# Optimization experiments

Hardware: AMD Instinct MI355X
Metric: run time of the kernel (lower is better)

Reference implementation:

```python
import jax, jax.numpy as jnp
import numpy as np

NH, HS, K = 32, 2048, 16
HD = HS // NH
B, L = 4, 2048
EPS = 1e-6

def _ln(x, gamma, beta):
    mu = x.mean(-1, keepdims=True)
    var = x.var(-1, keepdims=True)  # ddof=0 == torch unbiased=False
    return gamma * ((x - mu) / jnp.sqrt(var + EPS)) + beta

def _ln_fused_l2_bwd(x, target, gamma, beta):
    D = x.shape[-1]
    mu = x.mean(-1, keepdims=True)
    std = jnp.sqrt(x.var(-1, keepdims=True) + EPS)
    xh = (x - mu) / std
    gxh = (gamma * xh + beta - target) * gamma
    return (D * gxh - gxh.sum(-1, keepdims=True) - xh * (gxh * xh).sum(-1, keepdims=True)) / (D * std)

def setup_inputs() -> dict:
    key = jax.random.key(0)
    ks = jax.random.split(key, 8)
    s = 0.02
    return {
        'hidden_states': jax.random.normal(ks[0], (B, L, HS), jnp.float32),
        'position_ids': jnp.tile(jnp.arange(L, dtype=jnp.int32)[None], (B, 1)),
        'q_w': jax.random.normal(ks[1], (HS, HS), jnp.float32) * s,
        'k_w': jax.random.normal(ks[2], (HS, HS), jnp.float32) * s,
        'v_w': jax.random.normal(ks[3], (HS, HS), jnp.float32) * s,
        'o_w': jax.random.normal(ks[4], (HS, HS), jnp.float32) * s,
        'W1': jax.random.normal(ks[5], (NH, HD, HD), jnp.float32) * s,
        'b1': jnp.zeros((NH, 1, HD), jnp.float32),
        'ttt_norm_weight': jnp.ones((NH, HD), jnp.float32),
        'ttt_norm_bias': jnp.zeros((NH, HD), jnp.float32),
        'ttt_lr_weight': jax.random.normal(ks[6], (NH, 1, HS), jnp.float32) * s,
        'ttt_lr_bias': jnp.zeros((NH, 1), jnp.float32),
        'learnable_token_idx': jnp.zeros((K,), jnp.float32),
        'post_norm_weight': jnp.ones((HS,), jnp.float32),
        'post_norm_bias': jnp.zeros((HS,), jnp.float32),
    }

def _forward(hidden_states, q_w, k_w, v_w, o_w, W1, b1, ttt_norm_weight,
             ttt_norm_bias, ttt_lr_weight, ttt_lr_bias, learnable_token_idx,
             post_norm_weight, post_norm_bias):
    Bb, Ll, _ = hidden_states.shape
    NM = Ll // K

    def proj_heads(w):
        return (hidden_states @ w.T).reshape(Bb, Ll, NH, HD).transpose(0, 2, 1, 3)

    XQ = proj_heads(q_w).reshape(Bb, NH, NM, K, HD)
    XK = proj_heads(k_w).reshape(Bb, NH, NM, K, HD)
    XV = proj_heads(v_w).reshape(Bb, NH, NM, K, HD)
    X = hidden_states.reshape(Bb, NM, K, HS)

    # eta: learned per-token lr gate, [B,nh,NM,K,K]
    ttt_lr = jnp.einsum('bnkc,hdc->bhnkd', X, ttt_lr_weight) + ttt_lr_bias.reshape(1, NH, 1, 1, 1)
    ttt_lr_eta = jax.nn.sigmoid(ttt_lr).transpose(0, 1, 2, 4, 3) / HD  # ttt_base_lr = 1.0
    token_idx = jnp.clip(1.0 / jnp.arange(1, K + 1, dtype=jnp.float32) + learnable_token_idx, 0.0, None)
    eta = token_idx.reshape(1, 1, 1, K, 1) * ttt_lr_eta

    ln_w = ttt_norm_weight.reshape(NH, 1, HD)
    ln_b = ttt_norm_bias.reshape(NH, 1, HD)

    def step(carry, x):
        W1_s, b1_s = carry                 # [B,nh,hd,hd], [B,nh,1,hd]
        xq, xk, xv, eta_mb = x             # [B,nh,K,hd], eta_mb [B,nh,K,K]
        Z1 = xk @ W1_s + b1_s
        grad = _ln_fused_l2_bwd(Z1, xv - xk, ln_w, ln_b)
        Attn1 = jnp.tril(xq @ xk.swapaxes(-1, -2))
        b1_bar = b1_s - jnp.tril(eta_mb) @ grad
        Z1_bar = xq @ W1_s - (eta_mb * Attn1) @ grad + b1_bar
        last_eta = eta_mb[:, :, -1, :, None]  # [B,nh,K,1]
        W1_new = W1_s - (last_eta * xk).swapaxes(-1, -2) @ grad
        b1_new = b1_s - jnp.sum(last_eta * grad, axis=-2, keepdims=True)
        out = xq + _ln(Z1_bar, ln_w, ln_b)
        return (W1_new, b1_new), out

    init = (jnp.tile(W1[None], (Bb, 1, 1, 1)), jnp.tile(b1[None], (Bb, 1, 1, 1)))
    xs = (XQ.transpose(2, 0, 1, 3, 4), XK.transpose(2, 0, 1, 3, 4),
          XV.transpose(2, 0, 1, 3, 4), eta.transpose(2, 0, 1, 3, 4))
    _, ys = jax.lax.scan(step, init, xs)          # [NM,B,nh,K,hd]
    out = ys.transpose(1, 0, 3, 2, 4).reshape(Bb, Ll, HS)
    out = _ln(out, post_norm_weight, post_norm_bias)  # post_norm (eps 1e-6)
    return out @ o_w.T

def reference(hidden_states, position_ids, q_w, k_w, v_w, o_w, W1, b1,
              ttt_norm_weight, ttt_norm_bias, ttt_lr_weight, ttt_lr_bias,
              learnable_token_idx, post_norm_weight, post_norm_bias):
    del position_ids  # unused in the shown forward (rope never applied)
    return _forward(hidden_states, q_w, k_w, v_w, o_w, W1, b1, ttt_norm_weight,
                    ttt_norm_bias, ttt_lr_weight, ttt_lr_bias, learnable_token_idx,
                    post_norm_weight, post_norm_bias)
```

## Files before the change

kernel.cpp:

```cpp
#include <hip/hip_runtime.h>

typedef unsigned short u16;
typedef unsigned int u32;
typedef __bf16 bf16_t;
typedef bf16_t bf16x8 __attribute__((ext_vector_type(8)));
typedef float f32x4 __attribute__((ext_vector_type(4)));
typedef u16 u16x8 __attribute__((ext_vector_type(8)));

#define B_   4
#define L_   2048
#define HS_  2048
#define NH_  32
#define HD_  64
#define KK_  16
#define NM_  128
#define M_   (B_*L_)

__device__ __forceinline__ u16 f2bf(float f) {
  unsigned u = __float_as_uint(f);
  u += 0x7FFFu + ((u >> 16) & 1u);
  return (u16)(u >> 16);
}
__device__ __forceinline__ float bf2f(u16 u) {
  return __uint_as_float(((unsigned)u) << 16);
}
__device__ __forceinline__ f32x4 vshfl_xor(f32x4 v, int m) {
  f32x4 r;
  r[0] = __shfl_xor(v[0], m, 64); r[1] = __shfl_xor(v[1], m, 64);
  r[2] = __shfl_xor(v[2], m, 64); r[3] = __shfl_xor(v[3], m, 64);
  return r;
}

__global__ __launch_bounds__(256) void cast_f32_bf16(const float* __restrict__ in,
                                                     u16* __restrict__ out, int n) {
  int i = (blockIdx.x * 256 + threadIdx.x) * 8;
  if (i >= n) return;
  float4 a = *(const float4*)(in + i);
  float4 b = *(const float4*)(in + i + 4);
  u16x8 o;
  o[0]=f2bf(a.x); o[1]=f2bf(a.y); o[2]=f2bf(a.z); o[3]=f2bf(a.w);
  o[4]=f2bf(b.x); o[5]=f2bf(b.y); o[6]=f2bf(b.z); o[7]=f2bf(b.w);
  *(u16x8*)(out + i) = o;
}

#define BM 128
#define BN 128
#define BK 32
#define LDT 40

template <bool BF16OUT>
__global__ __launch_bounds__(256) void gemm_nt(const u16* __restrict__ A,
                                               const u16* __restrict__ Bt,
                                               void* __restrict__ Cv,
                                               int M, int N, int K) {
  __shared__ u16 As[BM * LDT];
  __shared__ u16 Bs[BN * LDT];
  int tid  = threadIdx.x;
  int lane = tid & 63, wave = tid >> 6;
  int quad = lane >> 4, l16 = lane & 15;
  int bM = blockIdx.x * BM, bN = blockIdx.y * BN;
  int wM = (wave >> 1) * 64, wN = (wave & 1) * 64;
  int r0 = tid >> 2, c0 = (tid & 3) * 8;
  const u16* Ap = A + (size_t)bM * K;
  const u16* Bp = Bt + (size_t)bN * K;
  f32x4 acc[4][4] = {};
  u16x8 pa0 = *(const u16x8*)(Ap + (size_t)r0 * K + c0);
  u16x8 pa1 = *(const u16x8*)(Ap + (size_t)(r0 + 64) * K + c0);
  u16x8 pb0 = *(const u16x8*)(Bp + (size_t)r0 * K + c0);
  u16x8 pb1 = *(const u16x8*)(Bp + (size_t)(r0 + 64) * K + c0);
  int nk = K / BK;
  for (int kt = 0; kt < nk; ++kt) {
    *(u16x8*)&As[r0 * LDT + c0]        = pa0;
    *(u16x8*)&As[(r0 + 64) * LDT + c0] = pa1;
    *(u16x8*)&Bs[r0 * LDT + c0]        = pb0;
    *(u16x8*)&Bs[(r0 + 64) * LDT + c0] = pb1;
    __syncthreads();
    if (kt + 1 < nk) {
      int k0 = (kt + 1) * BK + c0;
      pa0 = *(const u16x8*)(Ap + (size_t)r0 * K + k0);
      pa1 = *(const u16x8*)(Ap + (size_t)(r0 + 64) * K + k0);
      pb0 = *(const u16x8*)(Bp + (size_t)r0 * K + k0);
      pb1 = *(const u16x8*)(Bp + (size_t)(r0 + 64) * K + k0);
    }
    bf16x8 af[4], bfr[4];
#pragma unroll
    for (int i = 0; i < 4; ++i) {
      u16x8 t = *(const u16x8*)&As[(wM + i * 16 + l16) * LDT + quad * 8];
      af[i] = __builtin_bit_cast(bf16x8, t);
    }
#pragma unroll
    for (int j = 0; j < 4; ++j) {
      u16x8 t = *(const u16x8*)&Bs[(wN + j * 16 + l16) * LDT + quad * 8];
      bfr[j] = __builtin_bit_cast(bf16x8, t);
    }
#pragma unroll
    for (int i = 0; i < 4; ++i) {
#pragma unroll
      for (int j = 0; j < 4; ++j)
        acc[i][j] = __builtin_amdgcn_mfma_f32_16x16x32_bf16(af[i], bfr[j], acc[i][j], 0, 0, 0);
    }
    __syncthreads();
  }
#pragma unroll
  for (int i = 0; i < 4; ++i) {
#pragma unroll
    for (int j = 0; j < 4; ++j) {
      int row = bM + wM + i * 16 + quad * 4;
      int col = bN + wN + j * 16 + l16;
      if (BF16OUT) {
        u16* cp = (u16*)Cv + (size_t)row * N + col;
#pragma unroll
        for (int r = 0; r < 4; ++r) cp[(size_t)r * N] = f2bf(acc[i][j][r]);
      } else {
        float* cp = (float*)Cv + (size_t)row * N + col;
#pragma unroll
        for (int r = 0; r < 4; ++r) cp[(size_t)r * N] = acc[i][j][r];
      }
    }
  }
}

__global__ __launch_bounds__(256) void sig_kernel(const u16* __restrict__ hsb,
                                                  const u16* __restrict__ lrwb,
                                                  const float* __restrict__ lrb,
                                                  float* __restrict__ Sig) {
  __shared__ u16 Bs[32 * LDT];
  int tid = threadIdx.x;
  int lane = tid & 63, wave = tid >> 6;
  int quad = lane >> 4, l16 = lane & 15;
  int m0 = blockIdx.x * 64 + wave * 16;
  f32x4 acc0 = {}, acc1 = {};
  for (int kt = 0; kt < HS_ / BK; ++kt) {
    int k0 = kt * BK;
    if (tid < 128) {
      int r = tid >> 2, c8 = (tid & 3) * 8;
      *(u16x8*)&Bs[r * LDT + c8] = *(const u16x8*)(lrwb + (size_t)r * HS_ + k0 + c8);
    }
    __syncthreads();
    u16x8 ta = *(const u16x8*)(hsb + (size_t)(m0 + l16) * HS_ + k0 + quad * 8);
    u16x8 t0 = *(const u16x8*)&Bs[l16 * LDT + quad * 8];
    u16x8 t1 = *(const u16x8*)&Bs[(16 + l16) * LDT + quad * 8];
    bf16x8 af  = __builtin_bit_cast(bf16x8, ta);
    bf16x8 bf0 = __builtin_bit_cast(bf16x8, t0);
    bf16x8 bf1 = __builtin_bit_cast(bf16x8, t1);
    acc0 = __builtin_amdgcn_mfma_f32_16x16x32_bf16(af, bf0, acc0, 0, 0, 0);
    acc1 = __builtin_amdgcn_mfma_f32_16x16x32_bf16(af, bf1, acc1, 0, 0, 0);
    __syncthreads();
  }
#pragma unroll
  for (int j = 0; j < 2; ++j) {
    f32x4 a = j ? acc1 : acc0;
    int h = j * 16 + l16;
    float bias = lrb[h];
#pragma unroll
    for (int r = 0; r < 4; ++r) {
      int m = m0 + quad * 4 + r;
      float v = a[r] + bias;
      float s = (1.f / (1.f + expf(-v))) * (1.f / 64.f);
      Sig[(size_t)m * NH_ + h] = s;
    }
  }
}

__global__ __launch_bounds__(64, 1) void ttt_scan_wave(
    const u16* __restrict__ XQ, const u16* __restrict__ XK, const u16* __restrict__ XV,
    const float* __restrict__ Sig, const float* __restrict__ W1_0, const float* __restrict__ b1_0,
    const float* __restrict__ lnw, const float* __restrict__ lnb, const float* __restrict__ lti,
    float* __restrict__ Y) {
  __shared__ u16 W1t[64 * 72];
  __shared__ u16 gradT[64 * 40];
  __shared__ u16 coefA[16 * 40];
  __shared__ u16 xkT[64 * 40];
  __shared__ float diffS[16 * 68];
  __shared__ float xqF[16 * 68];

  int lane = threadIdx.x;
  int quad = lane >> 4, l16 = lane & 15;
  int bh = blockIdx.x, b = bh >> 5, h = bh & 31;

  {
    u32* p = (u32*)gradT; for (int i = lane; i < 1280; i += 64) p[i] = 0;
    u32* q = (u32*)coefA; for (int i = lane; i < 320;  i += 64) q[i] = 0;
    u32* s = (u32*)xkT;   for (int i = lane; i < 1280; i += 64) s[i] = 0;
  }

  f32x4 master[4][4];
  {
    const float* wsrc = W1_0 + (size_t)h * 4096;
#pragma unroll
    for (int c = 0; c < 4; ++c) {
      const float* wc = wsrc + (size_t)(c * 16 + l16) * 64 + quad * 4;
#pragma unroll
      for (int a = 0; a < 4; ++a)
#pragma unroll
        for (int r = 0; r < 4; ++r) master[a][c][r] = wc[a * 16 + r];
    }
  }
#pragma unroll
  for (int a = 0; a < 4; ++a)
#pragma unroll
    for (int c = 0; c < 4; ++c)
#pragma unroll
      for (int r = 0; r < 4; ++r)
        W1t[(a * 16 + quad * 4 + r) * 72 + c * 16 + l16] = f2bf(master[a][c][r]);

  f32x4 b1r, gam, bet;
#pragma unroll
  for (int c = 0; c < 4; ++c) {
    b1r[c] = b1_0[h * 64 + c * 16 + l16];
    gam[c] = lnw[h * 64 + c * 16 + l16];
    bet[c] = lnb[h * 64 + c * 16 + l16];
  }
  f32x4 tok4;
#pragma unroll
  for (int r = 0; r < 4; ++r) {
    int kk = quad * 4 + r;
    tok4[r] = fmaxf(1.0f / (float)(kk + 1) + lti[kk], 0.0f);
  }
  float tok15 = fmaxf(1.0f / 16.0f + lti[15], 0.0f);

  size_t gb  = ((size_t)(b * L_ + l16)) * HS_ + h * HD_ + quad * 8;
  size_t sgb = (size_t)(b * L_ + l16) * NH_ + h;

  u16x8 cxk[2], cxq[2], cxv[2];
  float csig;
#pragma unroll
  for (int kc = 0; kc < 2; ++kc) {
    cxk[kc] = *(const u16x8*)(XK + gb + kc * 32);
    cxq[kc] = *(const u16x8*)(XQ + gb + kc * 32);
    cxv[kc] = *(const u16x8*)(XV + gb + kc * 32);
  }
  csig = Sig[sgb];

  for (int n = 0; n < NM_; ++n) {
    bf16x8 fw[4][2];
#pragma unroll
    for (int cb = 0; cb < 4; ++cb)
#pragma unroll
      for (int kc = 0; kc < 2; ++kc)
        fw[cb][kc] = __builtin_bit_cast(bf16x8,
            *(const u16x8*)&W1t[(cb * 16 + l16) * 72 + kc * 32 + quad * 8]);

#pragma unroll
    for (int kc = 0; kc < 2; ++kc) {
      float dv[8], qv[8];
#pragma unroll
      for (int j = 0; j < 8; ++j) {
        dv[j] = bf2f(cxv[kc][j]) - bf2f(cxk[kc][j]);
        qv[j] = bf2f(cxq[kc][j]);
      }
      float4 d0 = {dv[0], dv[1], dv[2], dv[3]}, d1 = {dv[4], dv[5], dv[6], dv[7]};
      float4 q0 = {qv[0], qv[1], qv[2], qv[3]}, q1 = {qv[4], qv[5], qv[6], qv[7]};
      *(float4*)&diffS[l16 * 68 + kc * 32 + quad * 8]     = d0;
      *(float4*)&diffS[l16 * 68 + kc * 32 + quad * 8 + 4] = d1;
      *(float4*)&xqF[l16 * 68 + kc * 32 + quad * 8]       = q0;
      *(float4*)&xqF[l16 * 68 + kc * 32 + quad * 8 + 4]   = q1;
#pragma unroll
      for (int j = 0; j < 8; ++j)
        xkT[(kc * 32 + quad * 8 + j) * 40 + l16] = f2bf(-tok15 * bf2f(cxk[kc][j]));
    }
    f32x4 ssig;
#pragma unroll
    for (int r = 0; r < 4; ++r) ssig[r] = __shfl(csig, quad * 4 + r, 64);

    bf16x8 fxk[2], fxq[2];
#pragma unroll
    for (int kc = 0; kc < 2; ++kc) {
      fxk[kc] = __builtin_bit_cast(bf16x8, cxk[kc]);
      fxq[kc] = __builtin_bit_cast(bf16x8, cxq[kc]);
    }

    if (n + 1 < NM_) {
      size_t g = gb + (size_t)(n + 1) * KK_ * HS_;
#pragma unroll
      for (int kc = 0; kc < 2; ++kc) {
        cxk[kc] = *(const u16x8*)(XK + g + kc * 32);
        cxq[kc] = *(const u16x8*)(XQ + g + kc * 32);
        cxv[kc] = *(const u16x8*)(XV + g + kc * 32);
      }
      csig = Sig[sgb + (size_t)(n + 1) * KK_ * NH_];
    }

    f32x4 z1[4] = {}, zq[4] = {}, at = {};
#pragma unroll
    for (int kc = 0; kc < 2; ++kc) {
      at = __builtin_amdgcn_mfma_f32_16x16x32_bf16(fxq[kc], fxk[kc], at, 0, 0, 0);
#pragma unroll
      for (int cb = 0; cb < 4; ++cb) {
        z1[cb] = __builtin_amdgcn_mfma_f32_16x16x32_bf16(fxk[kc], fw[cb][kc], z1[cb], 0, 0, 0);
        zq[cb] = __builtin_amdgcn_mfma_f32_16x16x32_bf16(fxq[kc], fw[cb][kc], zq[cb], 0, 0, 0);
      }
    }

#pragma unroll
    for (int r = 0; r < 4; ++r) {
      int kk = quad * 4 + r;
      float cc = (l16 <= kk) ? tok4[r] * (1.0f + at[r]) : 0.0f;
      coefA[kk * 40 + l16] = f2bf(-cc);
    }

    f32x4 dd[4], xqr[4];
#pragma unroll
    for (int cb = 0; cb < 4; ++cb)
#pragma unroll
      for (int r = 0; r < 4; ++r) {
        dd[cb][r]  = diffS[(quad * 4 + r) * 68 + cb * 16 + l16];
        xqr[cb][r] = xqF[(quad * 4 + r) * 68 + cb * 16 + l16];
      }

    f32x4 s1 = {}, s2 = {};
#pragma unroll
    for (int cb = 0; cb < 4; ++cb) {
#pragma unroll
      for (int r = 0; r < 4; ++r) z1[cb][r] += b1r[cb];
      s1 = s1 + z1[cb];
      s2 = s2 + z1[cb] * z1[cb];
    }
#pragma unroll
    for (int m = 1; m <= 8; m <<= 1) { s1 = s1 + vshfl_xor(s1, m); s2 = s2 + vshfl_xor(s2, m); }
    f32x4 mu, rstd;
#pragma unroll
    for (int r = 0; r < 4; ++r) {
      mu[r] = s1[r] * (1.0f / 64.0f);
      float var = s2[r] * (1.0f / 64.0f) - mu[r] * mu[r];
      rstd[r] = 1.0f / sqrtf(var + 1e-6f);
    }

    f32x4 xh[4], gxh[4], t1v = {}, t2v = {};
#pragma unroll
    for (int cb = 0; cb < 4; ++cb) {
#pragma unroll
      for (int r = 0; r < 4; ++r) {
        xh[cb][r]  = (z1[cb][r] - mu[r]) * rstd[r];
        gxh[cb][r] = (gam[cb] * xh[cb][r] + bet[cb] - dd[cb][r]) * gam[cb];
      }
      t1v = t1v + gxh[cb];
      t2v = t2v + gxh[cb] * xh[cb];
    }
#pragma unroll
    for (int m = 1; m <= 8; m <<= 1) { t1v = t1v + vshfl_xor(t1v, m); t2v = t2v + vshfl_xor(t2v, m); }

    f32x4 bsum = {};
#pragma unroll
    for (int cb = 0; cb < 4; ++cb) {
      float sg[4];
#pragma unroll
      for (int r = 0; r < 4; ++r) {
        float g = (64.0f * gxh[cb][r] - t1v[r] - xh[cb][r] * t2v[r]) * (rstd[r] * (1.0f / 64.0f));
        sg[r] = ssig[r] * g;
      }
      u32 p0 = (u32)f2bf(sg[0]) | ((u32)f2bf(sg[1]) << 16);
      u32 p1 = (u32)f2bf(sg[2]) | ((u32)f2bf(sg[3]) << 16);
      *(u32*)&gradT[(cb * 16 + l16) * 40 + quad * 4]     = p0;
      *(u32*)&gradT[(cb * 16 + l16) * 40 + quad * 4 + 2] = p1;
      bsum[cb] = sg[0] + sg[1] + sg[2] + sg[3];
    }
    bsum = bsum + vshfl_xor(bsum, 16);
    bsum = bsum + vshfl_xor(bsum, 32);

    bf16x8 fA = __builtin_bit_cast(bf16x8, *(const u16x8*)&coefA[l16 * 40 + quad * 8]);
    bf16x8 fG[4], fX[4];
#pragma unroll
    for (int cb = 0; cb < 4; ++cb) {
      fG[cb] = __builtin_bit_cast(bf16x8, *(const u16x8*)&gradT[(cb * 16 + l16) * 40 + quad * 8]);
      fX[cb] = __builtin_bit_cast(bf16x8, *(const u16x8*)&xkT[(cb * 16 + l16) * 40 + quad * 8]);
    }

    f32x4 zb[4];
#pragma unroll
    for (int cb = 0; cb < 4; ++cb) {
      zb[cb] = __builtin_amdgcn_mfma_f32_16x16x32_bf16(fA, fG[cb], zq[cb], 0, 0, 0);
#pragma unroll
      for (int r = 0; r < 4; ++r) zb[cb][r] += b1r[cb];
    }

#pragma unroll
    for (int a = 0; a < 4; ++a)
#pragma unroll
      for (int c = 0; c < 4; ++c)
        master[a][c] = __builtin_amdgcn_mfma_f32_16x16x32_bf16(fG[a], fX[c], master[a][c], 0, 0, 0);
#pragma unroll
    for (int c = 0; c < 4; ++c) b1r[c] -= tok15 * bsum[c];

    f32x4 w1s = {}, w2s = {};
#pragma unroll
    for (int cb = 0; cb < 4; ++cb) { w1s = w1s + zb[cb]; w2s = w2s + zb[cb] * zb[cb]; }
#pragma unroll
    for (int m = 1; m <= 8; m <<= 1) { w1s = w1s + vshfl_xor(w1s, m); w2s = w2s + vshfl_xor(w2s, m); }
#pragma unroll
    for (int r = 0; r < 4; ++r) {
      float mu2 = w1s[r] * (1.0f / 64.0f);
      float var2 = w2s[r] * (1.0f / 64.0f) - mu2 * mu2;
      float rstd2 = 1.0f / sqrtf(var2 + 1e-6f);
      float* yp = Y + ((size_t)(b * L_ + n * KK_ + quad * 4 + r)) * HS_ + h * HD_ + l16;
#pragma unroll
      for (int cb = 0; cb < 4; ++cb)
        yp[cb * 16] = xqr[cb][r] + gam[cb] * ((zb[cb][r] - mu2) * rstd2) + bet[cb];
    }

#pragma unroll
    for (int a = 0; a < 4; ++a)
#pragma unroll
      for (int c = 0; c < 4; ++c)
#pragma unroll
        for (int r = 0; r < 4; ++r)
          W1t[(a * 16 + quad * 4 + r) * 72 + c * 16 + l16] = f2bf(master[a][c][r]);
  }
}

__global__ __launch_bounds__(256) void postnorm(const float* __restrict__ Yin,
                                                const float* __restrict__ w,
                                                const float* __restrict__ bb,
                                                u16* __restrict__ Yn) {
  __shared__ float red[8];
  int row = blockIdx.x, tid = threadIdx.x;
  const float* x = Yin + (size_t)row * HS_ + tid * 8;
  float4 v0 = *(const float4*)(x);
  float4 v1 = *(const float4*)(x + 4);
  float s  = v0.x + v0.y + v0.z + v0.w + v1.x + v1.y + v1.z + v1.w;
  float ss = v0.x*v0.x + v0.y*v0.y + v0.z*v0.z + v0.w*v0.w
           + v1.x*v1.x + v1.y*v1.y + v1.z*v1.z + v1.w*v1.w;
#pragma unroll
  for (int m = 32; m > 0; m >>= 1) { s += __shfl_xor(s, m, 64); ss += __shfl_xor(ss, m, 64); }
  int wave = tid >> 6, lane = tid & 63;
  if (lane == 0) { red[wave] = s; red[4 + wave] = ss; }
  __syncthreads();
  float S  = red[0] + red[1] + red[2] + red[3];
  float SS = red[4] + red[5] + red[6] + red[7];
  float mu = S * (1.f / 2048.f);
  float var = SS * (1.f / 2048.f) - mu * mu;
  float rstd = 1.f / sqrtf(var + 1e-6f);
  const float* wp = w + tid * 8;
  const float* bp = bb + tid * 8;
  float vals[8] = {v0.x, v0.y, v0.z, v0.w, v1.x, v1.y, v1.z, v1.w};
  u16x8 o;
#pragma unroll
  for (int t = 0; t < 8; ++t) o[t] = f2bf(wp[t] * ((vals[t] - mu) * rstd) + bp[t]);
  *(u16x8*)(Yn + (size_t)row * HS_ + tid * 8) = o;
}

extern "C" void kernel_launch(void* const* d_in, const int* in_sizes, int n_in,
                              void* d_out, int out_size, void* d_ws, size_t ws_size,
                              hipStream_t stream) {
  (void)in_sizes; (void)n_in; (void)out_size; (void)ws_size;
  const float* hidden = (const float*)d_in[0];
  const float* q_w = (const float*)d_in[2];
  const float* k_w = (const float*)d_in[3];
  const float* v_w = (const float*)d_in[4];
  const float* o_w = (const float*)d_in[5];
  const float* W1  = (const float*)d_in[6];
  const float* b1i = (const float*)d_in[7];
  const float* lnw = (const float*)d_in[8];
  const float* lnb = (const float*)d_in[9];
  const float* lrw = (const float*)d_in[10];
  const float* lrb = (const float*)d_in[11];
  const float* lti = (const float*)d_in[12];
  const float* pnw = (const float*)d_in[13];
  const float* pnb = (const float*)d_in[14];
  float* out = (float*)d_out;

  char* w = (char*)d_ws;
  u16* hsb  = (u16*)w;  w += (size_t)16777216 * 2;
  u16* wb   = (u16*)w;  w += (size_t)4194304 * 2;
  u16* lrwb = (u16*)w;  w += (size_t)65536 * 2;
  u16* XQb  = (u16*)w;  w += (size_t)16777216 * 2;
  u16* XKb  = (u16*)w;  w += (size_t)16777216 * 2;
  u16* XVb  = (u16*)w;  w += (size_t)16777216 * 2;
  float* Sg = (float*)w; w += (size_t)M_ * NH_ * 4;
  u16* Yn = hsb;

  cast_f32_bf16<<<8192, 256, 0, stream>>>(hidden, hsb, 16777216);
  cast_f32_bf16<<<32, 256, 0, stream>>>(lrw, lrwb, 65536);

  sig_kernel<<<128, 256, 0, stream>>>(hsb, lrwb, lrb, Sg);

  dim3 gg(M_ / BM, HS_ / BN);
  cast_f32_bf16<<<2048, 256, 0, stream>>>(q_w, wb, 4194304);
  gemm_nt<true><<<gg, 256, 0, stream>>>(hsb, wb, XQb, M_, HS_, HS_);
  cast_f32_bf16<<<2048, 256, 0, stream>>>(k_w, wb, 4194304);
  gemm_nt<true><<<gg, 256, 0, stream>>>(hsb, wb, XKb, M_, HS_, HS_);
  cast_f32_bf16<<<2048, 256, 0, stream>>>(v_w, wb, 4194304);
  gemm_nt<true><<<gg, 256, 0, stream>>>(hsb, wb, XVb, M_, HS_, HS_);

  ttt_scan_wave<<<128, 64, 0, stream>>>(XQb, XKb, XVb, Sg, W1, b1i, lnw, lnb, lti, out);

  postnorm<<<8192, 256, 0, stream>>>(out, pnw, pnb, Yn);

  cast_f32_bf16<<<2048, 256, 0, stream>>>(o_w, wb, 4194304);
  gemm_nt<false><<<gg, 256, 0, stream>>>(Yn, wb, out, M_, HS_, HS_);
}
```

Baseline: 1.053 ms.

## Keep TTT scan state in registers with 16x16x16 MFMA layout and DPP reductions

Result: faster. 893.0 us (-15.2%).

```diff
diff --git a/kernel.cpp b/kernel.cpp
--- a/kernel.cpp
+++ b/kernel.cpp
@@ -3,9 +3,12 @@
 typedef unsigned short u16;
 typedef unsigned int u32;
 typedef __bf16 bf16_t;
+typedef bf16_t bf16x4 __attribute__((ext_vector_type(4)));
 typedef bf16_t bf16x8 __attribute__((ext_vector_type(8)));
 typedef float f32x4 __attribute__((ext_vector_type(4)));
+typedef u16 u16x4 __attribute__((ext_vector_type(4)));
 typedef u16 u16x8 __attribute__((ext_vector_type(8)));
+typedef short s16x4 __attribute__((ext_vector_type(4)));
 
 #define B_   4
 #define L_   2048
@@ -24,11 +27,38 @@
 __device__ __forceinline__ float bf2f(u16 u) {
   return __uint_as_float(((unsigned)u) << 16);
 }
-__device__ __forceinline__ f32x4 vshfl_xor(f32x4 v, int m) {
+__device__ __forceinline__ u16 f2bfh(float f) {
+  __bf16 h = (__bf16)f;
+  return __builtin_bit_cast(u16, h);
+}
+__device__ __forceinline__ s16x4 pk4(float a, float b, float c, float d) {
+  bf16x4 v;
+  v[0] = (__bf16)a; v[1] = (__bf16)b; v[2] = (__bf16)c; v[3] = (__bf16)d;
+  return __builtin_bit_cast(s16x4, v);
+}
+
+__device__ __forceinline__ f32x4 mfma16(s16x4 a, s16x4 b, f32x4 c) {
+  return __builtin_amdgcn_mfma_f32_16x16x16bf16_1k(a, b, c, 0, 0, 0);
+}
+
+template <int CTRL>
+__device__ __forceinline__ float dpp_add(float v) {
+  int t = __builtin_amdgcn_update_dpp(0, __builtin_bit_cast(int, v), CTRL, 0xF, 0xF, true);
+  return v + __builtin_bit_cast(float, t);
+}
+template <int CTRL>
+__device__ __forceinline__ f32x4 dpp_add4(f32x4 v) {
   f32x4 r;
-  r[0] = __shfl_xor(v[0], m, 64); r[1] = __shfl_xor(v[1], m, 64);
-  r[2] = __shfl_xor(v[2], m, 64); r[3] = __shfl_xor(v[3], m, 64);
+#pragma unroll
+  for (int i = 0; i < 4; ++i) r[i] = dpp_add<CTRL>(v[i]);
   return r;
+}
+__device__ __forceinline__ f32x4 row_reduce16(f32x4 v) {
+  v = dpp_add4<0x121>(v);
+  v = dpp_add4<0x122>(v);
+  v = dpp_add4<0x124>(v);
+  v = dpp_add4<0x128>(v);
+  return v;
 }
 
 __global__ __launch_bounds__(256) void cast_f32_bf16(const float* __restrict__ in,
@@ -167,157 +197,114 @@
     const float* __restrict__ Sig, const float* __restrict__ W1_0, const float* __restrict__ b1_0,
     const float* __restrict__ lnw, const float* __restrict__ lnb, const float* __restrict__ lti,
     float* __restrict__ Y) {
-  __shared__ u16 W1t[64 * 72];
-  __shared__ u16 gradT[64 * 40];
-  __shared__ u16 coefA[16 * 40];
-  __shared__ u16 xkT[64 * 40];
-  __shared__ float diffS[16 * 68];
-  __shared__ float xqF[16 * 68];
+  __shared__ __align__(16) u16 xkT[64 * 20];
+  __shared__ __align__(16) float diffS[16 * 68];
 
   int lane = threadIdx.x;
   int quad = lane >> 4, l16 = lane & 15;
   int bh = blockIdx.x, b = bh >> 5, h = bh & 31;
 
-  {
-    u32* p = (u32*)gradT; for (int i = lane; i < 1280; i += 64) p[i] = 0;
-    u32* q = (u32*)coefA; for (int i = lane; i < 320;  i += 64) q[i] = 0;
-    u32* s = (u32*)xkT;   for (int i = lane; i < 1280; i += 64) s[i] = 0;
-  }
-
-  f32x4 master[4][4];
+  f32x4 m2[4][4];
   {
     const float* wsrc = W1_0 + (size_t)h * 4096;
 #pragma unroll
+    for (int c = 0; c < 4; ++c)
+#pragma unroll
+      for (int a = 0; a < 4; ++a)
+#pragma unroll
+        for (int r = 0; r < 4; ++r)
+          m2[c][a][r] = wsrc[(size_t)(c * 16 + quad * 4 + r) * 64 + a * 16 + l16];
+  }
+
+  f32x4 b1r, gam, bet;
+#pragma unroll
+  for (int a = 0; a < 4; ++a) {
+    b1r[a] = b1_0[h * 64 + a * 16 + l16];
+    gam[a] = lnw[h * 64 + a * 16 + l16];
+    bet[a] = lnb[h * 64 + a * 16 + l16];
+  }
+  float tokL  = fmaxf(1.0f / (float)(l16 + 1) + lti[l16], 0.0f);
+  float tok15 = fmaxf(1.0f / 16.0f + lti[15], 0.0f);
+
+  size_t gb = ((size_t)(b * L_ + l16)) * HS_ + h * HD_ + quad * 4;
+  const float* sigp = Sig + (size_t)(b * L_ + quad * 4) * NH_ + h;
+
+  u16x4 cxk[4], cxq[4], cxv[4];
+  f32x4 csig;
+#pragma unroll
+  for (int c = 0; c < 4; ++c) {
+    cxk[c] = *(const u16x4*)(XK + gb + c * 16);
+    cxq[c] = *(const u16x4*)(XQ + gb + c * 16);
+    cxv[c] = *(const u16x4*)(XV + gb + c * 16);
+  }
+#pragma unroll
+  for (int r = 0; r < 4; ++r) csig[r] = sigp[(size_t)r * NH_];
+
+  for (int n = 0; n < NM_; ++n) {
+    s16x4 fwB[4][4];
+#pragma unroll
+    for (int c = 0; c < 4; ++c)
+#pragma unroll
+      for (int a = 0; a < 4; ++a)
+        fwB[c][a] = pk4(m2[c][a][0], m2[c][a][1], m2[c][a][2], m2[c][a][3]);
+
+#pragma unroll
     for (int c = 0; c < 4; ++c) {
-      const float* wc = wsrc + (size_t)(c * 16 + l16) * 64 + quad * 4;
-#pragma unroll
-      for (int a = 0; a < 4; ++a)
-#pragma unroll
-        for (int r = 0; r < 4; ++r) master[a][c][r] = wc[a * 16 + r];
-    }
-  }
-#pragma unroll
-  for (int a = 0; a < 4; ++a)
-#pragma unroll
-    for (int c = 0; c < 4; ++c)
-#pragma unroll
-      for (int r = 0; r < 4; ++r)
-        W1t[(a * 16 + quad * 4 + r) * 72 + c * 16 + l16] = f2bf(master[a][c][r]);
-
-  f32x4 b1r, gam, bet;
-#pragma unroll
-  for (int c = 0; c < 4; ++c) {
-    b1r[c] = b1_0[h * 64 + c * 16 + l16];
-    gam[c] = lnw[h * 64 + c * 16 + l16];
-    bet[c] = lnb[h * 64 + c * 16 + l16];
-  }
-  f32x4 tok4;
-#pragma unroll
-  for (int r = 0; r < 4; ++r) {
-    int kk = quad * 4 + r;
-    tok4[r] = fmaxf(1.0f / (float)(kk + 1) + lti[kk], 0.0f);
-  }
-  float tok15 = fmaxf(1.0f / 16.0f + lti[15], 0.0f);
-
-  size_t gb  = ((size_t)(b * L_ + l16)) * HS_ + h * HD_ + quad * 8;
-  size_t sgb = (size_t)(b * L_ + l16) * NH_ + h;
-
-  u16x8 cxk[2], cxq[2], cxv[2];
-  float csig;
-#pragma unroll
-  for (int kc = 0; kc < 2; ++kc) {
-    cxk[kc] = *(const u16x8*)(XK + gb + kc * 32);
-    cxq[kc] = *(const u16x8*)(XQ + gb + kc * 32);
-    cxv[kc] = *(const u16x8*)(XV + gb + kc * 32);
-  }
-  csig = Sig[sgb];
-
-  for (int n = 0; n < NM_; ++n) {
-    bf16x8 fw[4][2];
-#pragma unroll
-    for (int cb = 0; cb < 4; ++cb)
-#pragma unroll
-      for (int kc = 0; kc < 2; ++kc)
-        fw[cb][kc] = __builtin_bit_cast(bf16x8,
-            *(const u16x8*)&W1t[(cb * 16 + l16) * 72 + kc * 32 + quad * 8]);
-
-#pragma unroll
-    for (int kc = 0; kc < 2; ++kc) {
-      float dv[8], qv[8];
-#pragma unroll
-      for (int j = 0; j < 8; ++j) {
-        dv[j] = bf2f(cxv[kc][j]) - bf2f(cxk[kc][j]);
-        qv[j] = bf2f(cxq[kc][j]);
-      }
-      float4 d0 = {dv[0], dv[1], dv[2], dv[3]}, d1 = {dv[4], dv[5], dv[6], dv[7]};
-      float4 q0 = {qv[0], qv[1], qv[2], qv[3]}, q1 = {qv[4], qv[5], qv[6], qv[7]};
-      *(float4*)&diffS[l16 * 68 + kc * 32 + quad * 8]     = d0;
-      *(float4*)&diffS[l16 * 68 + kc * 32 + quad * 8 + 4] = d1;
-      *(float4*)&xqF[l16 * 68 + kc * 32 + quad * 8]       = q0;
-      *(float4*)&xqF[l16 * 68 + kc * 32 + quad * 8 + 4]   = q1;
-#pragma unroll
-      for (int j = 0; j < 8; ++j)
-        xkT[(kc * 32 + quad * 8 + j) * 40 + l16] = f2bf(-tok15 * bf2f(cxk[kc][j]));
-    }
-    f32x4 ssig;
-#pragma unroll
-    for (int r = 0; r < 4; ++r) ssig[r] = __shfl(csig, quad * 4 + r, 64);
-
-    bf16x8 fxk[2], fxq[2];
-#pragma unroll
-    for (int kc = 0; kc < 2; ++kc) {
-      fxk[kc] = __builtin_bit_cast(bf16x8, cxk[kc]);
-      fxq[kc] = __builtin_bit_cast(bf16x8, cxq[kc]);
-    }
+      f32x4 dv;
+#pragma unroll
+      for (int j = 0; j < 4; ++j) dv[j] = bf2f(cxv[c][j]) - bf2f(cxk[c][j]);
+      *(f32x4*)&diffS[l16 * 68 + c * 16 + quad * 4] = dv;
+#pragma unroll
+      for (int j = 0; j < 4; ++j)
+        xkT[(c * 16 + quad * 4 + j) * 20 + l16] = f2bfh(-tok15 * bf2f(cxk[c][j]));
+    }
+
+    s16x4 fxk[4], fxq[4];
+#pragma unroll
+    for (int c = 0; c < 4; ++c) {
+      fxk[c] = __builtin_bit_cast(s16x4, cxk[c]);
+      fxq[c] = __builtin_bit_cast(s16x4, cxq[c]);
+    }
+    f32x4 sigc = csig;
 
     if (n + 1 < NM_) {
       size_t g = gb + (size_t)(n + 1) * KK_ * HS_;
 #pragma unroll
-      for (int kc = 0; kc < 2; ++kc) {
-        cxk[kc] = *(const u16x8*)(XK + g + kc * 32);
-        cxq[kc] = *(const u16x8*)(XQ + g + kc * 32);
-        cxv[kc] = *(const u16x8*)(XV + g + kc * 32);
+      for (int c = 0; c < 4; ++c) {
+        cxk[c] = *(const u16x4*)(XK + g + c * 16);
+        cxq[c] = *(const u16x4*)(XQ + g + c * 16);
+        cxv[c] = *(const u16x4*)(XV + g + c * 16);
       }
-      csig = Sig[sgb + (size_t)(n + 1) * KK_ * NH_];
-    }
-
-    f32x4 z1[4] = {}, zq[4] = {}, at = {};
-#pragma unroll
-    for (int kc = 0; kc < 2; ++kc) {
-      at = __builtin_amdgcn_mfma_f32_16x16x32_bf16(fxq[kc], fxk[kc], at, 0, 0, 0);
-#pragma unroll
-      for (int cb = 0; cb < 4; ++cb) {
-        z1[cb] = __builtin_amdgcn_mfma_f32_16x16x32_bf16(fxk[kc], fw[cb][kc], z1[cb], 0, 0, 0);
-        zq[cb] = __builtin_amdgcn_mfma_f32_16x16x32_bf16(fxq[kc], fw[cb][kc], zq[cb], 0, 0, 0);
+#pragma unroll
+      for (int r = 0; r < 4; ++r)
+        csig[r] = sigp[(size_t)((n + 1) * KK_ + r) * NH_];
+    }
+
+    f32x4 z1[4] = {}, zq4[4] = {}, atT = {};
+#pragma unroll
+    for (int c = 0; c < 4; ++c) {
+      atT = mfma16(fxk[c], fxq[c], atT);
+#pragma unroll
+      for (int a = 0; a < 4; ++a) {
+        z1[a]  = mfma16(fxk[c], fwB[c][a], z1[a]);
+        zq4[a] = mfma16(fxq[c], fwB[c][a], zq4[a]);
       }
     }
 
-#pragma unroll
-    for (int r = 0; r < 4; ++r) {
-      int kk = quad * 4 + r;
-      float cc = (l16 <= kk) ? tok4[r] * (1.0f + at[r]) : 0.0f;
-      coefA[kk * 40 + l16] = f2bf(-cc);
-    }
-
-    f32x4 dd[4], xqr[4];
-#pragma unroll
-    for (int cb = 0; cb < 4; ++cb)
-#pragma unroll
-      for (int r = 0; r < 4; ++r) {
-        dd[cb][r]  = diffS[(quad * 4 + r) * 68 + cb * 16 + l16];
-        xqr[cb][r] = xqF[(quad * 4 + r) * 68 + cb * 16 + l16];
-      }
-
-    f32x4 s1 = {}, s2 = {};
-#pragma unroll
-    for (int cb = 0; cb < 4; ++cb) {
-#pragma unroll
-      for (int r = 0; r < 4; ++r) z1[cb][r] += b1r[cb];
-      s1 = s1 + z1[cb];
-      s2 = s2 + z1[cb] * z1[cb];
-    }
-#pragma unroll
-    for (int m = 1; m <= 8; m <<= 1) { s1 = s1 + vshfl_xor(s1, m); s2 = s2 + vshfl_xor(s2, m); }
+    float cf[4];
+#pragma unroll
+    for (int r = 0; r < 4; ++r)
+      cf[r] = (quad * 4 + r <= l16) ? -tokL * (1.0f + atT[r]) : 0.0f;
+    s16x4 fA = pk4(cf[0], cf[1], cf[2], cf[3]);
+
+#pragma unroll
+    for (int a = 0; a < 4; ++a)
+#pragma unroll
+      for (int r = 0; r < 4; ++r) z1[a][r] += b1r[a];
+    f32x4 s1 = z1[0] + z1[1] + z1[2] + z1[3];
+    f32x4 s2 = z1[0] * z1[0] + z1[1] * z1[1] + z1[2] * z1[2] + z1[3] * z1[3];
+    s1 = row_reduce16(s1);
+    s2 = row_reduce16(s2);
     f32x4 mu, rstd;
 #pragma unroll
     for (int r = 0; r < 4; ++r) {
@@ -326,67 +313,72 @@
       rstd[r] = 1.0f / sqrtf(var + 1e-6f);
     }
 
+    f32x4 dd[4];
+#pragma unroll
+    for (int a = 0; a < 4; ++a)
+#pragma unroll
+      for (int r = 0; r < 4; ++r)
+        dd[a][r] = diffS[(quad * 4 + r) * 68 + a * 16 + l16];
+
     f32x4 xh[4], gxh[4], t1v = {}, t2v = {};
 #pragma unroll
-    for (int cb = 0; cb < 4; ++cb) {
+    for (int a = 0; a < 4; ++a) {
 #pragma unroll
       for (int r = 0; r < 4; ++r) {
-        xh[cb][r]  = (z1[cb][r] - mu[r]) * rstd[r];
-        gxh[cb][r] = (gam[cb] * xh[cb][r] + bet[cb] - dd[cb][r]) * gam[cb];
+        xh[a][r]  = (z1[a][r] - mu[r]) * rstd[r];
+        gxh[a][r] = (gam[a] * xh[a][r] + bet[a] - dd[a][r]) * gam[a];
       }
-      t1v = t1v + gxh[cb];
-      t2v = t2v + gxh[cb] * xh[cb];
-    }
-#pragma unroll
-    for (int m = 1; m <= 8; m <<= 1) { t1v = t1v + vshfl_xor(t1v, m); t2v = t2v + vshfl_xor(t2v, m); }
-
-    f32x4 bsum = {};
-#pragma unroll
-    for (int cb = 0; cb < 4; ++cb) {
+      t1v = t1v + gxh[a];
+      t2v = t2v + gxh[a] * xh[a];
+    }
+    t1v = row_reduce16(t1v);
+    t2v = row_reduce16(t2v);
+
+    s16x4 fG[4];
+    float bs[4];
+#pragma unroll
+    for (int a = 0; a < 4; ++a) {
       float sg[4];
 #pragma unroll
       for (int r = 0; r < 4; ++r) {
-        float g = (64.0f * gxh[cb][r] - t1v[r] - xh[cb][r] * t2v[r]) * (rstd[r] * (1.0f / 64.0f));
-        sg[r] = ssig[r] * g;
+        float g = (64.0f * gxh[a][r] - t1v[r] - xh[a][r] * t2v[r]) * (rstd[r] * (1.0f / 64.0f));
+        sg[r] = sigc[r] * g;
       }
-      u32 p0 = (u32)f2bf(sg[0]) | ((u32)f2bf(sg[1]) << 16);
-      u32 p1 = (u32)f2bf(sg[2]) | ((u32)f2bf(sg[3]) << 16);
-      *(u32*)&gradT[(cb * 16 + l16) * 40 + quad * 4]     = p0;
-      *(u32*)&gradT[(cb * 16 + l16) * 40 + quad * 4 + 2] = p1;
-      bsum[cb] = sg[0] + sg[1] + sg[2] + sg[3];
-    }
-    bsum = bsum + vshfl_xor(bsum, 16);
-    bsum = bsum + vshfl_xor(bsum, 32);
-
-    bf16x8 fA = __builtin_bit_cast(bf16x8, *(const u16x8*)&coefA[l16 * 40 + quad * 8]);
-    bf16x8 fG[4], fX[4];
-#pragma unroll
-    for (int cb = 0; cb < 4; ++cb) {
-      fG[cb] = __builtin_bit_cast(bf16x8, *(const u16x8*)&gradT[(cb * 16 + l16) * 40 + quad * 8]);
-      fX[cb] = __builtin_bit_cast(bf16x8, *(const u16x8*)&xkT[(cb * 16 + l16) * 40 + quad * 8]);
+      fG[a] = pk4(sg[0], sg[1], sg[2], sg[3]);
+      bs[a] = sg[0] + sg[1] + sg[2] + sg[3];
+    }
+#pragma unroll
+    for (int a = 0; a < 4; ++a) {
+      bs[a] += __shfl_xor(bs[a], 16, 64);
+      bs[a] += __shfl_xor(bs[a], 32, 64);
     }
 
     f32x4 zb[4];
 #pragma unroll
-    for (int cb = 0; cb < 4; ++cb) {
-      zb[cb] = __builtin_amdgcn_mfma_f32_16x16x32_bf16(fA, fG[cb], zq[cb], 0, 0, 0);
-#pragma unroll
-      for (int r = 0; r < 4; ++r) zb[cb][r] += b1r[cb];
-    }
-
-#pragma unroll
-    for (int a = 0; a < 4; ++a)
+    for (int a = 0; a < 4; ++a) {
+      zb[a] = mfma16(fA, fG[a], zq4[a]);
+#pragma unroll
+      for (int r = 0; r < 4; ++r) zb[a][r] += b1r[a];
+    }
+#pragma unroll
+    for (int a = 0; a < 4; ++a) b1r[a] -= tok15 * bs[a];
+
+    {
+      s16x4 fX[4];
 #pragma unroll
       for (int c = 0; c < 4; ++c)
-        master[a][c] = __builtin_amdgcn_mfma_f32_16x16x32_bf16(fG[a], fX[c], master[a][c], 0, 0, 0);
-#pragma unroll
-    for (int c = 0; c < 4; ++c) b1r[c] -= tok15 * bsum[c];
-
-    f32x4 w1s = {}, w2s = {};
-#pragma unroll
-    for (int cb = 0; cb < 4; ++cb) { w1s = w1s + zb[cb]; w2s = w2s + zb[cb] * zb[cb]; }
-#pragma unroll
-    for (int m = 1; m <= 8; m <<= 1) { w1s = w1s + vshfl_xor(w1s, m); w2s = w2s + vshfl_xor(w2s, m); }
+        fX[c] = *(const s16x4*)&xkT[(c * 16 + l16) * 20 + quad * 4];
+#pragma unroll
+      for (int c = 0; c < 4; ++c)
+#pragma unroll
+        for (int a = 0; a < 4; ++a)
+          m2[c][a] = mfma16(fX[c], fG[a], m2[c][a]);
+    }
+
+    f32x4 w1s = zb[0] + zb[1] + zb[2] + zb[3];
+    f32x4 w2s = zb[0] * zb[0] + zb[1] * zb[1] + zb[2] * zb[2] + zb[3] * zb[3];
+    w1s = row_reduce16(w1s);
+    w2s = row_reduce16(w2s);
 #pragma unroll
     for (int r = 0; r < 4; ++r) {
       float mu2 = w1s[r] * (1.0f / 64.0f);
@@ -394,21 +386,14 @@
       float rstd2 = 1.0f / sqrtf(var2 + 1e-6f);
       float* yp = Y + ((size_t)(b * L_ + n * KK_ + quad * 4 + r)) * HS_ + h * HD_ + l16;
 #pragma unroll
-      for (int cb = 0; cb < 4; ++cb)
-        yp[cb * 16] = xqr[cb][r] + gam[cb] * ((zb[cb][r] - mu2) * rstd2) + bet[cb];
-    }
-
-#pragma unroll
-    for (int a = 0; a < 4; ++a)
-#pragma unroll
-      for (int c = 0; c < 4; ++c)
-#pragma unroll
-        for (int r = 0; r < 4; ++r)
-          W1t[(a * 16 + quad * 4 + r) * 72 + c * 16 + l16] = f2bf(master[a][c][r]);
+      for (int a = 0; a < 4; ++a)
+        yp[a * 16] = gam[a] * ((zb[a][r] - mu2) * rstd2) + bet[a];
+    }
   }
 }
 
 __global__ __launch_bounds__(256) void postnorm(const float* __restrict__ Yin,
+                                                const u16* __restrict__ XQr,
                                                 const float* __restrict__ w,
                                                 const float* __restrict__ bb,
                                                 u16* __restrict__ Yn) {
@@ -417,9 +402,13 @@
   const float* x = Yin + (size_t)row * HS_ + tid * 8;
   float4 v0 = *(const float4*)(x);
   float4 v1 = *(const float4*)(x + 4);
-  float s  = v0.x + v0.y + v0.z + v0.w + v1.x + v1.y + v1.z + v1.w;
-  float ss = v0.x*v0.x + v0.y*v0.y + v0.z*v0.z + v0.w*v0.w
-           + v1.x*v1.x + v1.y*v1.y + v1.z*v1.z + v1.w*v1.w;
+  u16x8 xqv = *(const u16x8*)(XQr + (size_t)row * HS_ + tid * 8);
+  float vals[8] = {v0.x, v0.y, v0.z, v0.w, v1.x, v1.y, v1.z, v1.w};
+#pragma unroll
+  for (int t = 0; t < 8; ++t) vals[t] += bf2f(xqv[t]);
+  float s = 0.f, ss = 0.f;
+#pragma unroll
+  for (int t = 0; t < 8; ++t) { s += vals[t]; ss += vals[t] * vals[t]; }
 #pragma unroll
   for (int m = 32; m > 0; m >>= 1) { s += __shfl_xor(s, m, 64); ss += __shfl_xor(ss, m, 64); }
   int wave = tid >> 6, lane = tid & 63;
@@ -432,7 +421,6 @@
   float rstd = 1.f / sqrtf(var + 1e-6f);
   const float* wp = w + tid * 8;
   const float* bp = bb + tid * 8;
-  float vals[8] = {v0.x, v0.y, v0.z, v0.w, v1.x, v1.y, v1.z, v1.w};
   u16x8 o;
 #pragma unroll
   for (int t = 0; t < 8; ++t) o[t] = f2bf(wp[t] * ((vals[t] - mu) * rstd) + bp[t]);
@@ -484,7 +472,7 @@
 
   ttt_scan_wave<<<128, 64, 0, stream>>>(XQb, XKb, XVb, Sg, W1, b1i, lnw, lnb, lti, out);
 
-  postnorm<<<8192, 256, 0, stream>>>(out, pnw, pnb, Yn);
+  postnorm<<<8192, 256, 0, stream>>>(out, XQb, pnw, pnb, Yn);
 
   cast_f32_bf16<<<2048, 256, 0, stream>>>(o_w, wb, 4194304);
   gemm_nt<false><<<gg, 256, 0, stream>>>(Yn, wb, out, M_, HS_, HS_);
```
